# Optimization experiments

Measured on AMD Instinct MI355X. Metric: run time of the kernel, lower is better.

Reference implementation:

```python
import jax, jax.numpy as jnp
import numpy as np

N = 100000      # nodes
E = 3200000     # edges (before self loops)
F_IN = 5        # node_features
SH = 32         # spatial_hidden
H = 8           # heads
C = SH // H     # per-head dim = 4
TH = 64         # temporal_hidden
TC = TH // 3    # 21 (trend/seasonal lstm hidden)
TR = TH - 2 * TC  # 22 (residual mlp)
SEQ = 14
CV_THRESH = 1.5


def setup_inputs() -> dict:
    key = jax.random.key(0)
    cnt = [0]
    def nk():
        cnt[0] += 1
        return jax.random.fold_in(key, cnt[0])
    def nrm(shape, s=0.1):
        return jax.random.normal(nk(), shape, jnp.float32) * s
    inp = {}
    inp['x'] = nrm((N, F_IN), 1.0)
    inp['edge_index'] = jax.random.randint(nk(), (2, E), 0, N)
    inp['trend'] = nrm((1, SEQ), 1.0)
    inp['seasonal'] = nrm((1, SEQ), 1.0)
    inp['residual'] = nrm((1, SEQ), 1.0)
    inp['cv_values'] = jax.random.uniform(nk(), (1,), jnp.float32, 0.0, 3.0)
    inp['target_store_idx'] = 42
    # GAT layers: layer0 in=F_IN, layers 1,2 in=SH
    for i, din in enumerate([F_IN, SH, SH]):
        inp[f'gat_W{i}'] = nrm((din, SH), 1.0 / np.sqrt(din))
        inp[f'gat_as{i}'] = nrm((H, C))
        inp[f'gat_ad{i}'] = nrm((H, C))
        inp[f'gat_b{i}'] = jnp.zeros((SH,), jnp.float32)
    # two 2-layer LSTMs (input sizes 1 then TC), PyTorch gate order i,f,g,o
    for p in ('t', 's'):
        for l, din in enumerate([1, TC]):
            inp[f'{p}_Wih{l}'] = nrm((4 * TC, din), 1.0 / np.sqrt(TC))
            inp[f'{p}_Whh{l}'] = nrm((4 * TC, TC), 1.0 / np.sqrt(TC))
            inp[f'{p}_bih{l}'] = jnp.zeros((4 * TC,), jnp.float32)
            inp[f'{p}_bhh{l}'] = jnp.zeros((4 * TC,), jnp.float32)
    inp['res_W'] = nrm((1, TR), 1.0)
    inp['res_b'] = jnp.zeros((TR,), jnp.float32)
    FU = SH + TH  # 96
    inp['pg_W'] = nrm((FU + 1, FU), 1.0 / np.sqrt(FU))
    inp['pg_b'] = jnp.zeros((FU,), jnp.float32)
    inp['f1_W'] = nrm((FU, TH), 1.0 / np.sqrt(FU))
    inp['f1_b'] = jnp.zeros((TH,), jnp.float32)
    inp['ln_g'] = jnp.ones((TH,), jnp.float32)
    inp['ln_b'] = jnp.zeros((TH,), jnp.float32)
    inp['f2_W'] = nrm((TH, TH // 2), 1.0 / np.sqrt(TH))
    inp['f2_b'] = jnp.zeros((TH // 2,), jnp.float32)
    inp['f3_W'] = nrm((TH // 2, SEQ), 1.0 / np.sqrt(TH // 2))
    inp['f3_b'] = jnp.zeros((SEQ,), jnp.float32)
    return inp


def _gat(h_in, src, dst, W, a_s, a_d, b):
    # PyG GATConv: message src->dst, softmax over incoming edges per dst
    h = (h_in @ W).reshape(-1, H, C)            # [N,H,C]
    es = jnp.einsum('nhc,hc->nh', h, a_s)       # [N,H]
    ed = jnp.einsum('nhc,hc->nh', h, a_d)
    e = jax.nn.leaky_relu(es[src] + ed[dst], 0.2)  # [Etot,H]
    emax = jax.ops.segment_max(e, dst, num_segments=N)
    emax = jnp.where(jnp.isfinite(emax), emax, 0.0)
    a = jnp.exp(e - emax[dst])
    den = jax.ops.segment_sum(a, dst, num_segments=N)
    a = a / (den[dst] + 1e-16)
    out = jax.ops.segment_sum(h[src] * a[..., None], dst, num_segments=N)
    return out.reshape(-1, H * C) + b


def _lstm2(x, params):
    # x: [B,T,in]; params: list of (Wih[4h,in], Whh[4h,h], bih, bhh)
    seq = x
    for (Wih, Whh, bih, bhh) in params:
        B = seq.shape[0]
        hh = Whh.shape[1]
        def step(carry, xt):
            hprev, cprev = carry
            g = xt @ Wih.T + hprev @ Whh.T + bih + bhh
            i, f, gg, o = jnp.split(g, 4, axis=-1)
            c = jax.nn.sigmoid(f) * cprev + jax.nn.sigmoid(i) * jnp.tanh(gg)
            hn = jax.nn.sigmoid(o) * jnp.tanh(c)
            return (hn, c), hn
        init = (jnp.zeros((B, hh), seq.dtype), jnp.zeros((B, hh), seq.dtype))
        _, ys = jax.lax.scan(step, init, jnp.swapaxes(seq, 0, 1))
        seq = jnp.swapaxes(ys, 0, 1)
    return seq


def _forward(x, trend, seasonal, residual, cv_values,
             gat_params, lstm_t, lstm_s,
             res_W, res_b, pg_W, pg_b,
             f1_W, f1_b, ln_g, ln_b, f2_W, f2_b, f3_W, f3_b,
             edge_index, target_store_idx):
    loops = jnp.arange(N, dtype=edge_index.dtype)  # add_self_loops=True
    src = jnp.concatenate([edge_index[0], loops])
    dst = jnp.concatenate([edge_index[1], loops])
    h = x
    for (W, a_s, a_d, b) in gat_params:
        h = jax.nn.elu(_gat(h, src, dst, W, a_s, a_d, b))
    target_spatial = h[target_store_idx][None, :]          # [1,SH]
    trend_out = _lstm2(trend[..., None], lstm_t)[:, -1, :]      # [1,TC]
    seasonal_out = _lstm2(seasonal[..., None], lstm_s)[:, -1, :]
    res_out = jax.nn.relu(residual[..., None] @ res_W + res_b)[:, -1, :]  # [1,TR]
    temporal = jnp.concatenate([trend_out, seasonal_out, res_out], -1)    # [1,TH]
    combined = jnp.concatenate([target_spatial, temporal], -1)            # [1,96]
    gated_in = jnp.concatenate([combined, cv_values[:, None]], -1)        # [1,97]
    gate = jax.nn.sigmoid(gated_in @ pg_W + pg_b)
    gf = combined * gate
    h1 = gf @ f1_W + f1_b
    mu = h1.mean(-1, keepdims=True)
    var = h1.var(-1, keepdims=True)
    h1 = jax.nn.relu((h1 - mu) / jnp.sqrt(var + 1e-5) * ln_g + ln_b)
    h2 = jax.nn.relu(h1 @ f2_W + f2_b)
    return h2 @ f3_W + f3_b                                 # [1,SEQ]


def reference(x, edge_index, trend, seasonal, residual, cv_values, target_store_idx,
              gat_W0, gat_as0, gat_ad0, gat_b0,
              gat_W1, gat_as1, gat_ad1, gat_b1,
              gat_W2, gat_as2, gat_ad2, gat_b2,
              t_Wih0, t_Whh0, t_bih0, t_bhh0, t_Wih1, t_Whh1, t_bih1, t_bhh1,
              s_Wih0, s_Whh0, s_bih0, s_bhh0, s_Wih1, s_Whh1, s_bih1, s_bhh1,
              res_W, res_b, pg_W, pg_b,
              f1_W, f1_b, ln_g, ln_b, f2_W, f2_b, f3_W, f3_b):
    gat_params = [(gat_W0, gat_as0, gat_ad0, gat_b0),
                  (gat_W1, gat_as1, gat_ad1, gat_b1),
                  (gat_W2, gat_as2, gat_ad2, gat_b2)]
    lstm_t = [(t_Wih0, t_Whh0, t_bih0, t_bhh0), (t_Wih1, t_Whh1, t_bih1, t_bhh1)]
    lstm_s = [(s_Wih0, s_Whh0, s_bih0, s_bhh0), (s_Wih1, s_Whh1, s_bih1, s_bhh1)]
    return _forward(x, trend, seasonal, residual, cv_values,
                    gat_params, lstm_t, lstm_s,
                    res_W, res_b, pg_W, pg_b,
                    f1_W, f1_b, ln_g, ln_b, f2_W, f2_b, f3_W, f3_b,
                    edge_index, target_store_idx)
```

## Files before the change

### kernel.cpp

```cpp
#include <hip/hip_runtime.h>
#include <hip/hip_bf16.h>
#include <stdint.h>
#include <math.h>

#define NN   100000
#define EE   3200000
#define FIN  5
#define SHD  32
#define NH   8
#define TCH  21
#define TRH  22
#define SEQL 14

#define ECA   1024
#define ECL1  1024
#define ECB   16384
#define ECL2  8192
#define ECC   131072

#define BCHK2 4096
#define NBC2  ((EE + BCHK2 - 1) / BCHK2)
#define NBW   ((NN + 31) / 32)
#define NBWP  3200

typedef __hip_bfloat16 bf16;
typedef __attribute__((ext_vector_type(2))) float f32x2;

__device__ __forceinline__ float b2f(bf16 v) { return __bfloat162float(v); }
__device__ __forceinline__ float sigm(float x) { return 1.f / (1.f + __expf(-x)); }
__device__ __forceinline__ float ldw(const void* p, int i, int f) {
    return f ? ((const float*)p)[i] : __bfloat162float(((const bf16*)p)[i]);
}
__device__ __forceinline__ float relu_nan(float v) {
    return (v == v) ? ((v > 0.f) ? v : 0.f) : v;
}
__device__ __forceinline__ unsigned short f2b(float v) {
    bf16 b = __float2bfloat16(v);
    return *reinterpret_cast<unsigned short*>(&b);
}
__device__ __forceinline__ float cvf(float v) { return v; }
__device__ __forceinline__ float cvf(bf16 v) { return __bfloat162float(v); }
__device__ __forceinline__ void cp(float* dst, const void* src, int n,
                                   int t0, int stride, int f) {
    if (f) {
        const float* s = (const float*)src;
        for (int i = t0; i < n; i += stride) dst[i] = s[i];
    } else {
        const bf16* s = (const bf16*)src;
        for (int i = t0; i < n; i += stride) dst[i] = b2f(s[i]);
    }
}

__global__ void PatternAwareSTGAT_94489281309_kernel(const unsigned int* xw, int* flag,
        const void* as0, const void* b0, const void* as1, const void* b1,
        const void* as2, const void* b2, float* prm) {
    int tid = threadIdx.x;
    int sane = 0;
    for (int i = 0; i < 64; i++) {
        unsigned int lo = xw[i] & 0xFFFFu;
        int e = (int)((lo >> 7) & 0xFF);
        if (e >= 110 && e <= 135) sane++;
    }
    int f = (sane >= 32) ? 0 : 1;
    if (tid == 0) flag[0] = f;
    const void* asp[3] = {as0, as1, as2};
    const void* bp[3]  = {b0, b1, b2};
    for (int l = 0; l < 3; l++)
        prm[l * 64 + tid] = (tid < 32) ? ldw(asp[l], tid, f) : ldw(bp[l], tid - 32, f);
}

__global__ __launch_bounds__(256) void k_scan2(
        const int* __restrict__ ei, const unsigned* __restrict__ bm,
        const int* __restrict__ tgtp,
        int* __restrict__ es, int* __restrict__ edd,
        int* __restrict__ cnt, int* __restrict__ deg, int cap) {
    __shared__ unsigned sbm[NBWP];
    __shared__ int wsum[4];
    __shared__ int sbase;
    int tid = threadIdx.x;
    const bool useBm = (bm != nullptr);
    int tgtv = useBm ? -1 : tgtp[0];
    if (useBm) {
        const uint4* b4 = (const uint4*)bm;
        uint4* s4 = (uint4*)sbm;
        uint4 t0 = b4[tid];
        uint4 t1 = b4[tid + 256];
        uint4 t2 = (tid + 512 < NBWP / 4) ? b4[tid + 512] : make_uint4(0,0,0,0);
        uint4 t3 = (tid + 768 < NBWP / 4) ? b4[tid + 768] : make_uint4(0,0,0,0);
        s4[tid] = t0;
        s4[tid + 256] = t1;
        if (tid + 512 < NBWP / 4) s4[tid + 512] = t2;
        if (tid + 768 < NBWP / 4) s4[tid + 768] = t3;
    }
    __syncthreads();

    int e0 = blockIdx.x * BCHK2 + tid * 16;
    unsigned mask = 0;
    int dv[16];
    if (e0 < EE) {
        const int4* dd4 = (const int4*)(ei + EE + e0);
        int4 a = dd4[0];
        int4 b = dd4[1];
        int4 c = dd4[2];
        int4 d = dd4[3];
        dv[0]=a.x; dv[1]=a.y; dv[2]=a.z; dv[3]=a.w;
        dv[4]=b.x; dv[5]=b.y; dv[6]=b.z; dv[7]=b.w;
        dv[8]=c.x; dv[9]=c.y; dv[10]=c.z; dv[11]=c.w;
        dv[12]=d.x; dv[13]=d.y; dv[14]=d.z; dv[15]=d.w;
#pragma unroll
        for (int j = 0; j < 16; j++) {
            bool mm = useBm ? (((sbm[dv[j] >> 5] >> (dv[j] & 31)) & 1u) != 0u)
                            : (dv[j] == tgtv);
            if (mm) mask |= (1u << j);
        }
    }
    int m = __popc(mask);

    int lane = tid & 63, wv = tid >> 6;
    int pre = m;
#pragma unroll
    for (int off = 1; off < 64; off <<= 1) {
        int v = __shfl_up(pre, off, 64);
        if (lane >= off) pre += v;
    }
    if (lane == 63) wsum[wv] = pre;
    __syncthreads();
    int wbase = 0;
#pragma unroll
    for (int q = 0; q < 4; q++) if (q < wv) wbase += wsum[q];
    int myoff = wbase + pre - m;
    if (tid == 0) {
        int tot = wsum[0] + wsum[1] + wsum[2] + wsum[3];
        sbase = (tot > 0) ? atomicAdd(cnt, tot) : 0;
    }
    __syncthreads();
    if (m > 0) {
        int off = sbase + myoff;
#pragma unroll
        for (int j = 0; j < 16; j++) {
            if (mask & (1u << j)) {
                int e = e0 + j;
                int dval = dv[j];
                int s = ei[e];
                if (off < cap) { es[off] = s; edd[off] = dval; }
                if (deg) atomicAdd(&deg[dval], 1);
                off++;
            }
        }
    }
}

__global__ void k_mark1(const int* __restrict__ eA, const int* __restrict__ cA,
                        const int* __restrict__ tgtp,
                        unsigned* __restrict__ bm1, int* __restrict__ l1,
                        int* __restrict__ c1,
                        int* __restrict__ l3, int* __restrict__ c3) {
    int n = cA[0]; if (n > ECA) n = ECA;
    for (int i = threadIdx.x; i < n; i += 256) {
        int s = eA[i];
        unsigned bit = 1u << (s & 31);
        unsigned old = atomicOr(&bm1[s >> 5], bit);
        if (!(old & bit)) {
            int p = atomicAdd(c1, 1);
            if (p < ECL1) l1[p] = s;
        }
    }
    if (threadIdx.x == 0) {
        int t = tgtp[0];
        unsigned bit = 1u << (t & 31);
        unsigned old = atomicOr(&bm1[t >> 5], bit);
        if (!(old & bit)) {
            int p = atomicAdd(c1, 1);
            if (p < ECL1) l1[p] = t;
        }
        l3[0] = t; c3[0] = 1;
    }
}

__global__ void k_prefix(const int* __restrict__ list, const int* __restrict__ cp, int cap,
                         const int* __restrict__ deg, int* __restrict__ rstart,
                         unsigned* __restrict__ bmN, int* __restrict__ lN,
                         int* __restrict__ cN, int capN) {
    __shared__ int sdd[256];
    __shared__ int sbase;
    int n = cp[0]; if (n > cap) n = cap;
    if (threadIdx.x == 0) sbase = 0;
    __syncthreads();
    for (int b = 0; b < n; b += 256) {
        int i = b + threadIdx.x;
        int nd = (i < n) ? list[i] : -1;
        sdd[threadIdx.x] = (nd >= 0) ? deg[nd] : 0;
        __syncthreads();
        if (threadIdx.x == 0) {
            int acc = sbase;
            for (int j = 0; j < 256; j++) { int v = sdd[j]; sdd[j] = acc; acc += v; }
            sbase = acc;
        }
        __syncthreads();
        if (nd >= 0) rstart[nd] = sdd[threadIdx.x];
        __syncthreads();
    }
    if (bmN) {
        for (int i = threadIdx.x; i < n; i += 256) {
            int nd = list[i];
            unsigned bit = 1u << (nd & 31);
            unsigned old = atomicOr(&bmN[nd >> 5], bit);
            if (!(old & bit)) {
                int p = atomicAdd(cN, 1);
                if (p < capN) lN[p] = nd;
            }
        }
    }
}

__global__ __launch_bounds__(256) void k_scatter(const int* __restrict__ es,
                                                 const int* __restrict__ edd,
                                                 const int* __restrict__ cp, int cap,
                                                 const int* __restrict__ rstart,
                                                 int* __restrict__ fill, int* __restrict__ csr,
                                                 unsigned* __restrict__ bmN,
                                                 int* __restrict__ lN,
                                                 int* __restrict__ cN, int capN) {
    int m = cp[0]; if (m > cap) m = cap;
    for (int i = blockIdx.x * 256 + threadIdx.x; i < m; i += gridDim.x * 256) {
        int s = es[i], d = edd[i];
        int p = atomicAdd(&fill[d], 1);
        csr[rstart[d] + p] = s;
        if (bmN) {
            unsigned bit = 1u << (s & 31);
            unsigned old = atomicOr(&bmN[s >> 5], bit);
            if (!(old & bit)) {
                int q = atomicAdd(cN, 1);
                if (q < capN) lN[q] = s;
            }
        }
    }
}

__global__ void k_transform0(const void* x, const void* W, const void* ad_,
                             const int* flag, unsigned short* hWb, float* ed) {
    __shared__ float sW[FIN * SHD];
    __shared__ float sad[SHD];
    int tid = threadIdx.x;
    int f = flag[0];
    cp(sW, W, FIN * SHD, tid, 256, f);
    if (tid >= 192 && tid < 192 + SHD) sad[tid - 192] = ldw(ad_, tid - 192, f);
    __syncthreads();
    int n = blockIdx.x * 256 + tid;
    if (n >= NN) return;
    float xr[FIN];
    if (f) {
        const float* xp = (const float*)x + (size_t)n * FIN;
        for (int k = 0; k < FIN; k++) xr[k] = xp[k];
    } else {
        const bf16* xp = (const bf16*)x + (size_t)n * FIN;
        for (int k = 0; k < FIN; k++) xr[k] = b2f(xp[k]);
    }
    float o[SHD];
    for (int j = 0; j < SHD; j++) o[j] = 0.f;
    for (int k = 0; k < FIN; k++) {
        float xv = xr[k];
        for (int j = 0; j < SHD; j++) o[j] += xv * sW[k * SHD + j];
    }
    ushort4* row = (ushort4*)(hWb + (size_t)n * SHD);
    for (int q = 0; q < 8; q++) {
        ushort4 v; v.x = f2b(o[q*4]); v.y = f2b(o[q*4+1]); v.z = f2b(o[q*4+2]); v.w = f2b(o[q*4+3]);
        row[q] = v;
    }
    for (int h = 0; h < NH; h++) {
        float e2 = 0.f;
        for (int c = 0; c < 4; c++) e2 += o[h * 4 + c] * sad[h * 4 + c];
        ed[(size_t)n * NH + h] = e2;
    }
}

__global__ void k_transform1(const int* __restrict__ list, const int* __restrict__ cntp,
                             int cap,
                             const float* x, const void* W, const void* ad_,
                             const int* flag, unsigned short* hWb, float* ed) {
    __shared__ float sW[SHD * SHD];
    __shared__ float sad[SHD];
    int tid = threadIdx.x;
    int f = flag[0];
    cp(sW, W, SHD * SHD, tid, 256, f);
    if (tid >= 192 && tid < 192 + SHD) sad[tid - 192] = ldw(ad_, tid - 192, f);
    __syncthreads();
    int cnt = cntp[0]; if (cnt > cap) cnt = cap;
    int ii = blockIdx.x * 256 + tid;
    if (ii >= cnt) return;
    int n = list[ii];
    float xr[SHD];
    const float4* xp4 = (const float4*)(x + (size_t)n * SHD);
#pragma unroll
    for (int q = 0; q < 8; q++) {
        float4 v = xp4[q];
        xr[q*4] = v.x; xr[q*4+1] = v.y; xr[q*4+2] = v.z; xr[q*4+3] = v.w;
    }
    float o[SHD];
    for (int j = 0; j < SHD; j++) o[j] = 0.f;
    for (int k = 0; k < SHD; k++) {
        float xv = xr[k];
        for (int j = 0; j < SHD; j++) o[j] += xv * sW[k * SHD + j];
    }
    ushort4* row = (ushort4*)(hWb + (size_t)n * SHD);
    for (int q = 0; q < 8; q++) {
        ushort4 v; v.x = f2b(o[q*4]); v.y = f2b(o[q*4+1]); v.z = f2b(o[q*4+2]); v.w = f2b(o[q*4+3]);
        row[q] = v;
    }
    for (int h = 0; h < NH; h++) {
        float e2 = 0.f;
        for (int c = 0; c < 4; c++) e2 += o[h * 4 + c] * sad[h * 4 + c];
        ed[(size_t)n * NH + h] = e2;
    }
}

__global__ void k_aggregate(const int* __restrict__ list, const int* __restrict__ cntp,
                            int cap,
                            const int* __restrict__ rstart, const int* __restrict__ rdeg,
                            const int* __restrict__ csr,
                            const int* __restrict__ ovr, int ovrCap,
                            const unsigned short* __restrict__ hWb,
                            const float* __restrict__ ed,
                            const float* __restrict__ prm,
                            float* __restrict__ out) {
    int gid = blockIdx.x * 256 + threadIdx.x;
    int lane = threadIdx.x & 63;
    int cnt = cntp[0]; if (cnt > cap) cnt = cap;
    int idx = (gid >> 6) * 2 + (lane >> 5);
    if (idx >= cnt) return;
    int n = list[idx];
    int l32 = lane & 31;
    int h = l32 & 7, k = l32 >> 3;
    float4 asv = *(const float4*)(prm + h * 4);
    float ednh = ed[(size_t)n * NH + h];
    int base, deg;
    if (ovr) { base = 0; deg = ovr[0]; if (deg > ovrCap) deg = ovrCap; }
    else     { base = rstart[n]; deg = rdeg[n]; }
    float den = 0.f;
    f32x2 acc01 = {0.f, 0.f}, acc23 = {0.f, 0.f};
    int t = k;
    int s0 = -1, s1 = -1, s2 = -1, s3 = -1, s4 = -1, s5 = -1;
    if (t <= deg)      s0 = (t == 0) ? n : __builtin_nontemporal_load(csr + base + t - 1);
    if (t + 4 <= deg)  s1 = __builtin_nontemporal_load(csr + base + t + 3);
    if (t + 8 <= deg)  s2 = __builtin_nontemporal_load(csr + base + t + 7);
    if (t + 12 <= deg) s3 = __builtin_nontemporal_load(csr + base + t + 11);
    if (t + 16 <= deg) s4 = __builtin_nontemporal_load(csr + base + t + 15);
    if (t + 20 <= deg) s5 = __builtin_nontemporal_load(csr + base + t + 19);
    while (s0 >= 0) {
        uint2 hv0 = *(const uint2*)(hWb + (size_t)s0 * SHD + h * 4);
        bool b1 = (s1 >= 0), b2 = (s2 >= 0), b3 = (s3 >= 0), b4 = (s4 >= 0), b5 = (s5 >= 0);
        uint2 hv1, hv2, hv3, hv4, hv5;
        if (b1) hv1 = *(const uint2*)(hWb + (size_t)s1 * SHD + h * 4);
        if (b2) hv2 = *(const uint2*)(hWb + (size_t)s2 * SHD + h * 4);
        if (b3) hv3 = *(const uint2*)(hWb + (size_t)s3 * SHD + h * 4);
        if (b4) hv4 = *(const uint2*)(hWb + (size_t)s4 * SHD + h * 4);
        if (b5) hv5 = *(const uint2*)(hWb + (size_t)s5 * SHD + h * 4);
        int tn = t + 24;
        int p0 = -1, p1 = -1, p2 = -1, p3 = -1, p4 = -1, p5 = -1;
        if (tn <= deg)      p0 = __builtin_nontemporal_load(csr + base + tn - 1);
        if (tn + 4 <= deg)  p1 = __builtin_nontemporal_load(csr + base + tn + 3);
        if (tn + 8 <= deg)  p2 = __builtin_nontemporal_load(csr + base + tn + 7);
        if (tn + 12 <= deg) p3 = __builtin_nontemporal_load(csr + base + tn + 11);
        if (tn + 16 <= deg) p4 = __builtin_nontemporal_load(csr + base + tn + 15);
        if (tn + 20 <= deg) p5 = __builtin_nontemporal_load(csr + base + tn + 19);
        {
            f32x2 h01, h23;
            h01.x = __uint_as_float(hv0.x << 16);
            h01.y = __uint_as_float(hv0.x & 0xffff0000u);
            h23.x = __uint_as_float(hv0.y << 16);
            h23.y = __uint_as_float(hv0.y & 0xffff0000u);
            f32x2 d2 = h01 * (f32x2){asv.x, asv.y} + h23 * (f32x2){asv.z, asv.w};
            float e = d2.x + d2.y + ednh;
            e = fmaxf(e, 0.2f * e);
            float a = __expf(e);
            den += a;
            f32x2 av = {a, a};
            acc01 += av * h01;
            acc23 += av * h23;
        }
        if (b1) {
            f32x2 h01, h23;
            h01.x = __uint_as_float(hv1.x << 16);
            h01.y = __uint_as_float(hv1.x & 0xffff0000u);
            h23.x = __uint_as_float(hv1.y << 16);
            h23.y = __uint_as_float(hv1.y & 0xffff0000u);
            f32x2 d2 = h01 * (f32x2){asv.x, asv.y} + h23 * (f32x2){asv.z, asv.w};
            float e = d2.x + d2.y + ednh;
            e = fmaxf(e, 0.2f * e);
            float a = __expf(e);
            den += a;
            f32x2 av = {a, a};
            acc01 += av * h01;
            acc23 += av * h23;
        }
        if (b2) {
            f32x2 h01, h23;
            h01.x = __uint_as_float(hv2.x << 16);
            h01.y = __uint_as_float(hv2.x & 0xffff0000u);
            h23.x = __uint_as_float(hv2.y << 16);
            h23.y = __uint_as_float(hv2.y & 0xffff0000u);
            f32x2 d2 = h01 * (f32x2){asv.x, asv.y} + h23 * (f32x2){asv.z, asv.w};
            float e = d2.x + d2.y + ednh;
            e = fmaxf(e, 0.2f * e);
            float a = __expf(e);
            den += a;
            f32x2 av = {a, a};
            acc01 += av * h01;
            acc23 += av * h23;
        }
        if (b3) {
            f32x2 h01, h23;
            h01.x = __uint_as_float(hv3.x << 16);
            h01.y = __uint_as_float(hv3.x & 0xffff0000u);
            h23.x = __uint_as_float(hv3.y << 16);
            h23.y = __uint_as_float(hv3.y & 0xffff0000u);
            f32x2 d2 = h01 * (f32x2){asv.x, asv.y} + h23 * (f32x2){asv.z, asv.w};
            float e = d2.x + d2.y + ednh;
            e = fmaxf(e, 0.2f * e);
            float a = __expf(e);
            den += a;
            f32x2 av = {a, a};
            acc01 += av * h01;
            acc23 += av * h23;
        }
        if (b4) {
            f32x2 h01, h23;
            h01.x = __uint_as_float(hv4.x << 16);
            h01.y = __uint_as_float(hv4.x & 0xffff0000u);
            h23.x = __uint_as_float(hv4.y << 16);
            h23.y = __uint_as_float(hv4.y & 0xffff0000u);
            f32x2 d2 = h01 * (f32x2){asv.x, asv.y} + h23 * (f32x2){asv.z, asv.w};
            float e = d2.x + d2.y + ednh;
            e = fmaxf(e, 0.2f * e);
            float a = __expf(e);
            den += a;
            f32x2 av = {a, a};
            acc01 += av * h01;
            acc23 += av * h23;
        }
        if (b5) {
            f32x2 h01, h23;
            h01.x = __uint_as_float(hv5.x << 16);
            h01.y = __uint_as_float(hv5.x & 0xffff0000u);
            h23.x = __uint_as_float(hv5.y << 16);
            h23.y = __uint_as_float(hv5.y & 0xffff0000u);
            f32x2 d2 = h01 * (f32x2){asv.x, asv.y} + h23 * (f32x2){asv.z, asv.w};
            float e = d2.x + d2.y + ednh;
            e = fmaxf(e, 0.2f * e);
            float a = __expf(e);
            den += a;
            f32x2 av = {a, a};
            acc01 += av * h01;
            acc23 += av * h23;
        }
        s0 = p0; s1 = p1; s2 = p2; s3 = p3; s4 = p4; s5 = p5; t = tn;
    }
    for (int off = 16; off >= 8; off >>= 1) {
        den      += __shfl_down(den, off, 32);
        acc01.x  += __shfl_down(acc01.x, off, 32);
        acc01.y  += __shfl_down(acc01.y, off, 32);
        acc23.x  += __shfl_down(acc23.x, off, 32);
        acc23.y  += __shfl_down(acc23.y, off, 32);
    }
    if (k == 0) {
        float inv = 1.f / (den + 1e-16f);
        float4 bv = *(const float4*)(prm + 32 + h * 4);
        float v0 = acc01.x * inv + bv.x;
        float v1 = acc01.y * inv + bv.y;
        float v2 = acc23.x * inv + bv.z;
        float v3 = acc23.y * inv + bv.w;
        v0 = (v0 > 0.f) ? v0 : expm1f(v0);
        v1 = (v1 > 0.f) ? v1 : expm1f(v1);
        v2 = (v2 > 0.f) ? v2 : expm1f(v2);
        v3 = (v3 > 0.f) ? v3 : expm1f(v3);
        *(float4*)(out + (size_t)n * SHD + h * 4) = make_float4(v0, v1, v2, v3);
    }
}

template<typename T>
__device__ __forceinline__ void lstm_load_regs(
        const T* Wih0, const T* Whh0, const T* bih0, const T* bhh0,
        const T* Wih1, const T* Whh1, const T* bih1, const T* bhh1,
        const T* xin, int l, bool bl, float* xs,
        float& wa, float& ba, float& wb, float& bb, float& ba2, float& bb2,
        float* Wa, float* Wb, float* Ua, float* Va, float* Ub, float* Vb) {
#pragma unroll
    for (int t = 0; t < SEQL; t++) xs[t] = cvf(xin[t]);
    wa = cvf(Wih0[l]);
    ba = cvf(bih0[l]) + cvf(bhh0[l]);
    wb = bl ? cvf(Wih0[64 + l]) : 0.f;
    bb = bl ? (cvf(bih0[64 + l]) + cvf(bhh0[64 + l])) : 0.f;
    ba2 = cvf(bih1[l]) + cvf(bhh1[l]);
    bb2 = bl ? (cvf(bih1[64 + l]) + cvf(bhh1[64 + l])) : 0.f;
#pragma unroll
    for (int j = 0; j < 21; j++) {
        Wa[j] = cvf(Whh0[l * 21 + j]);
        Wb[j] = bl ? cvf(Whh0[(64 + l) * 21 + j]) : 0.f;
        Ua[j] = cvf(Wih1[l * 21 + j]);
        Va[j] = cvf(Whh1[l * 21 + j]);
        Ub[j] = bl ? cvf(Wih1[(64 + l) * 21 + j]) : 0.f;
        Vb[j] = bl ? cvf(Whh1[(64 + l) * 21 + j]) : 0.f;
    }
}

__device__ __forceinline__ void warm_sweep(const void* p, int nbytes, int t2) {
    const uint4* s = (const uint4*)p;
    int nv = nbytes >> 4;
    unsigned acc = 0;
    for (int i = t2; i < nv; i += 1024) {
        uint4 v0 = s[i];
        uint4 v1 = (i + 128 < nv) ? s[i + 128] : make_uint4(0,0,0,0);
        uint4 v2 = (i + 256 < nv) ? s[i + 256] : make_uint4(0,0,0,0);
        uint4 v3 = (i + 384 < nv) ? s[i + 384] : make_uint4(0,0,0,0);
        uint4 v4 = (i + 512 < nv) ? s[i + 512] : make_uint4(0,0,0,0);
        uint4 v5 = (i + 640 < nv) ? s[i + 640] : make_uint4(0,0,0,0);
        uint4 v6 = (i + 768 < nv) ? s[i + 768] : make_uint4(0,0,0,0);
        uint4 v7 = (i + 896 < nv) ? s[i + 896] : make_uint4(0,0,0,0);
        acc ^= v0.x ^ v1.x ^ v2.x ^ v3.x ^ v4.x ^ v5.x ^ v6.x ^ v7.x;
    }
    asm volatile("" :: "v"(acc));
}

template<typename T>
__device__ __forceinline__ float matvec_t(const T* W, const float* vin,
                                          float bias, int n, int col, int ncol) {
    float acc = bias;
    int k2 = 0;
    for (; k2 + 8 <= n; k2 += 8) {
        float w0 = cvf(W[(k2 + 0) * ncol + col]);
        float w1 = cvf(W[(k2 + 1) * ncol + col]);
        float w2 = cvf(W[(k2 + 2) * ncol + col]);
        float w3 = cvf(W[(k2 + 3) * ncol + col]);
        float w4 = cvf(W[(k2 + 4) * ncol + col]);
        float w5 = cvf(W[(k2 + 5) * ncol + col]);
        float w6 = cvf(W[(k2 + 6) * ncol + col]);
        float w7 = cvf(W[(k2 + 7) * ncol + col]);
        acc += vin[k2 + 0] * w0; acc += vin[k2 + 1] * w1;
        acc += vin[k2 + 2] * w2; acc += vin[k2 + 3] * w3;
        acc += vin[k2 + 4] * w4; acc += vin[k2 + 5] * w5;
        acc += vin[k2 + 6] * w6; acc += vin[k2 + 7] * w7;
    }
    for (; k2 < n; k2++) acc += vin[k2] * cvf(W[k2 * ncol + col]);
    return acc;
}
__device__ __forceinline__ float matvec(const void* W, const float* vin,
                                        float bias, int n, int col, int ncol, int f) {
    return f ? matvec_t<float>((const float*)W, vin, bias, n, col, ncol)
             : matvec_t<bf16>((const bf16*)W, vin, bias, n, col, ncol);
}

__global__ __launch_bounds__(256, 1)
void k_tail(const void* trend, const void* seasonal, const void* residual,
                       const void* cv, const int* tgtp,
                       const void* tWih0, const void* tWhh0, const void* tbih0, const void* tbhh0,
                       const void* tWih1, const void* tWhh1, const void* tbih1, const void* tbhh1,
                       const void* sWih0, const void* sWhh0, const void* sbih0, const void* sbhh0,
                       const void* sWih1, const void* sWhh1, const void* sbih1, const void* sbhh1,
                       const void* res_W, const void* res_b,
                       const void* pg_W, const void* pg_b,
                       const void* f1_W, const void* f1_b,
                       const void* ln_g, const void* ln_b,
                       const void* f2_W, const void* f2_b,
                       const void* f3_W, const void* f3_b,
                       const int* flag, const float* A, void* out) {
    __shared__ __align__(16) float SH1[2][24];
    __shared__ __align__(16) float SH2[2][24];
    __shared__ float comb[97];
    __shared__ float gf[96];
    __shared__ float h1v[64];
    __shared__ float h2s[32];
    __shared__ float sbias[336];
    __shared__ float stats[2];
    const int tid = threadIdx.x;
    const int f = flag[0];
    const int w = tid >> 6, l = tid & 63;

    if (tid < 96) {
        if (tid < 48) SH1[tid / 24][tid % 24] = 0.f;
        else { int u = tid - 48; SH2[u / 24][u % 24] = 0.f; }
    }
    __syncthreads();

    if (w < 2) {
        const void* Wih0 = w ? sWih0 : tWih0;
        const void* Whh0 = w ? sWhh0 : tWhh0;
        const void* bih0 = w ? sbih0 : tbih0;
        const void* bhh0 = w ? sbhh0 : tbhh0;
        const void* Wih1 = w ? sWih1 : tWih1;
        const void* Whh1 = w ? sWhh1 : tWhh1;
        const void* bih1 = w ? sbih1 : tbih1;
        const void* bhh1 = w ? sbhh1 : tbhh1;
        const void* xin  = w ? seasonal : trend;
        const bool bl = (l < 20);
        float xs[SEQL];
        float wa, ba, wb, bb, ba2, bb2;
        float Wa[21], Wb[21], Ua[21], Va[21], Ub[21], Vb[21];
        if (f) {
            lstm_load_regs<float>((const float*)Wih0, (const float*)Whh0,
                (const float*)bih0, (const float*)bhh0,
                (const float*)Wih1, (const float*)Whh1,
                (const float*)bih1, (const float*)bhh1,
                (const float*)xin, l, bl, xs, wa, ba, wb, bb, ba2, bb2,
                Wa, Wb, Ua, Va, Ub, Vb);
        } else {
            lstm_load_regs<bf16>((const bf16*)Wih0, (const bf16*)Whh0,
                (const bf16*)bih0, (const bf16*)bhh0,
                (const bf16*)Wih1, (const bf16*)Whh1,
                (const bf16*)bih1, (const bf16*)bhh1,
                (const bf16*)xin, l, bl, xs, wa, ba, wb, bb, ba2, bb2,
                Wa, Wb, Ua, Va, Ub, Vb);
        }
#pragma unroll
        for (int j = 0; j < 21; j++) {
            asm volatile("" : "+v"(Wa[j]), "+v"(Wb[j]));
            asm volatile("" : "+v"(Ua[j]), "+v"(Va[j]));
            asm volatile("" : "+v"(Ub[j]), "+v"(Vb[j]));
        }
#pragma unroll
        for (int t = 0; t < SEQL; t++) asm volatile("" : "+v"(xs[t]));
        asm volatile("" : "+v"(wa), "+v"(ba));
        asm volatile("" : "+v"(wb), "+v"(bb));
        asm volatile("" : "+v"(ba2), "+v"(bb2));

        float h1r = 0.f, c1v = 0.f, h2r = 0.f, c2v = 0.f;
#pragma unroll 1
        for (int t = 0; t < SEQL; t++) {
            float aa = ba + xs[t] * wa;
            float ab = bb + xs[t] * wb;
#pragma unroll
            for (int q = 0; q < 5; q++) {
                float4 v = *(const float4*)&SH1[w][q * 4];
                aa += v.x * Wa[q*4];   ab += v.x * Wb[q*4];
                aa += v.y * Wa[q*4+1]; ab += v.y * Wb[q*4+1];
                aa += v.z * Wa[q*4+2]; ab += v.z * Wb[q*4+2];
                aa += v.w * Wa[q*4+3]; ab += v.w * Wb[q*4+3];
            }
            { float v20 = SH1[w][20]; aa += v20 * Wa[20]; ab += v20 * Wb[20]; }
            float fj = __shfl(aa, 21 + l);
            float gj = __shfl(aa, 42 + l);
            float oa = __shfl(aa, 63);
            float ob = __shfl(ab, (l == 0) ? 0 : (l - 1));
            float oj = (l == 0) ? oa : ob;
            if (l < 21) {
                c1v = sigm(fj) * c1v + sigm(aa) * tanhf(gj);
                h1r = sigm(oj) * tanhf(c1v);
                SH1[w][l] = h1r;
            }
            __threadfence_block();
            float a2 = ba2, b2v = bb2;
#pragma unroll
            for (int q = 0; q < 5; q++) {
                float4 u = *(const float4*)&SH1[w][q * 4];
                float4 v = *(const float4*)&SH2[w][q * 4];
                a2  += u.x * Ua[q*4]   + v.x * Va[q*4];
                b2v += u.x * Ub[q*4]   + v.x * Vb[q*4];
                a2  += u.y * Ua[q*4+1] + v.y * Va[q*4+1];
                b2v += u.y * Ub[q*4+1] + v.y * Vb[q*4+1];
                a2  += u.z * Ua[q*4+2] + v.z * Va[q*4+2];
                b2v += u.z * Ub[q*4+2] + v.z * Vb[q*4+2];
                a2  += u.w * Ua[q*4+3] + v.w * Va[q*4+3];
                b2v += u.w * Ub[q*4+3] + v.w * Vb[q*4+3];
            }
            { float u20 = SH1[w][20], v20 = SH2[w][20];
              a2  += u20 * Ua[20] + v20 * Va[20];
              b2v += u20 * Ub[20] + v20 * Vb[20]; }
            float fj2 = __shfl(a2, 21 + l);
            float gj2 = __shfl(a2, 42 + l);
            float oa2 = __shfl(a2, 63);
            float ob2 = __shfl(b2v, (l == 0) ? 0 : (l - 1));
            float oj2 = (l == 0) ? oa2 : ob2;
            if (l < 21) {
                c2v = sigm(fj2) * c2v + sigm(a2) * tanhf(gj2);
                h2r = sigm(oj2) * tanhf(c2v);
                SH2[w][l] = h2r;
            }
            __threadfence_block();
        }
        if (l < 21) comb[(w == 0 ? 32 : 53) + l] = h2r;
    } else {
        int t2 = tid - 128;
        if (t2 < TRH)
            comb[74 + t2] = relu_nan(ldw(residual, SEQL - 1, f) * ldw(res_W, t2, f)
                                     + ldw(res_b, t2, f));
        if (t2 == TRH) comb[96] = ldw(cv, 0, f);
        if (t2 >= 32 && t2 < 64) {
            int tgt = tgtp[0];
            comb[t2 - 32] = A[(size_t)tgt * SHD + (t2 - 32)];
        }
        for (int i = t2; i < 336; i += 128) {
            float v;
            if (i < 96)       v = ldw(pg_b, i, f);
            else if (i < 160) v = ldw(f1_b, i - 96, f);
            else if (i < 192) v = ldw(f2_b, i - 160, f);
            else if (i < 206) v = ldw(f3_b, i - 192, f);
            else if (i < 208) v = 0.f;
            else if (i < 272) v = ldw(ln_g, i - 208, f);
            else              v = ldw(ln_b, i - 272, f);
            sbias[i] = v;
        }
        int esz = f ? 4 : 2;
        warm_sweep(pg_W, 9312 * esz, t2);
        warm_sweep(f1_W, 6144 * esz, t2);
        warm_sweep(f2_W, 2048 * esz, t2);
        warm_sweep(f3_W,  448 * esz, t2);
    }
    __syncthreads();

    if (tid < 96)
        gf[tid] = comb[tid] * sigm(matvec(pg_W, comb, sbias[tid], 97, tid, 96, f));
    __syncthreads();
    if (tid < 64)
        h1v[tid] = matvec(f1_W, gf, sbias[96 + tid], 96, tid, 64, f);
    __syncthreads();
    if (tid == 0) {
        float mu = 0.f;
        for (int j = 0; j < 64; j++) mu += h1v[j];
        mu /= 64.f;
        float var = 0.f;
        for (int j = 0; j < 64; j++) { float d = h1v[j] - mu; var += d * d; }
        var /= 64.f;
        stats[0] = mu; stats[1] = rsqrtf(var + 1e-5f);
    }
    __syncthreads();
    if (tid < 64)
        h1v[tid] = relu_nan((h1v[tid] - stats[0]) * stats[1] * sbias[208 + tid] + sbias[272 + tid]);
    __syncthreads();
    if (tid < 32)
        h2s[tid] = relu_nan(matvec(f2_W, h1v, sbias[160 + tid], 64, tid, 32, f));
    __syncthreads();
    if (tid < SEQL) {
        float acc = matvec(f3_W, h2s, sbias[192 + tid], 32, tid, 14, f);
        if (acc != acc) acc = 3333.0f;
        if (f) ((float*)out)[tid] = acc;
        else   ((bf16*)out)[tid] = __float2bfloat16(acc);
    }
}

static inline unsigned short h_f2bf(float f) {
    union { float f; unsigned u; } x; x.f = f;
    return (unsigned short)(x.u >> 16);
}
static unsigned short g_diag[SEQL];

extern "C" void kernel_launch(void* const* d_in, const int* in_sizes, int n_in,
                              void* d_out, int out_size, void* d_ws, size_t ws_size,
                              hipStream_t stream) {
    const int* ei  = (const int*)d_in[1];
    const int* tgt = (const int*)d_in[6];

    const size_t HWB  = sizeof(unsigned short) * (size_t)NN * SHD;
    const size_t EDB  = sizeof(float) * (size_t)NN * NH;
    const size_t AB   = sizeof(float) * (size_t)NN * SHD;
    const size_t ZER  = sizeof(int) * (size_t)(16 + 2 * NBWP + 4 * NN);
    const size_t RSTB = sizeof(int) * (size_t)(2 * NN);
    const size_t LSTB = sizeof(int) * (size_t)(2 * ECA + ECL1 + 8 + ECL2
                                               + 3 * ECB + 3 * ECC);
    const size_t NEED = 256 + 1024 + ZER + RSTB + LSTB + 512 + HWB + EDB + AB;
    if (ws_size < NEED) {
        for (int i = 0; i < SEQL; i++) g_diag[i] = h_f2bf(7777.0f);
        hipMemcpyAsync(d_out, g_diag, SEQL * sizeof(unsigned short),
                       hipMemcpyHostToDevice, stream);
        return;
    }

    char* p = (char*)d_ws;
    int*   flag = (int*)p;   p += 256;
    float* prm  = (float*)p; p += 1024;
    int* cnts  = (int*)p; p += sizeof(int) * 16;
    unsigned* bm1 = (unsigned*)p; p += sizeof(int) * NBWP;
    unsigned* bm2 = (unsigned*)p; p += sizeof(int) * NBWP;
    int* degB  = (int*)p; p += sizeof(int) * NN;
    int* fillB = (int*)p; p += sizeof(int) * NN;
    int* degC  = (int*)p; p += sizeof(int) * NN;
    int* fillC = (int*)p; p += sizeof(int) * NN;
    int* rstartB = (int*)p; p += sizeof(int) * NN;
    int* rstartC = (int*)p; p += sizeof(int) * NN;
    int* eA   = (int*)p; p += sizeof(int) * ECA;
    int* eAd  = (int*)p; p += sizeof(int) * ECA;
    int* l1   = (int*)p; p += sizeof(int) * ECL1;
    int* l3   = (int*)p; p += sizeof(int) * 8;
    int* l2   = (int*)p; p += sizeof(int) * ECL2;
    int* eBs  = (int*)p; p += sizeof(int) * ECB;
    int* eBd  = (int*)p; p += sizeof(int) * ECB;
    int* csrB = (int*)p; p += sizeof(int) * ECB;
    int* eCs  = (int*)p; p += sizeof(int) * ECC;
    int* eCd  = (int*)p; p += sizeof(int) * ECC;
    int* csrC = (int*)p; p += sizeof(int) * ECC;
    p = (char*)(((uintptr_t)p + 255) & ~(uintptr_t)255);
    unsigned short* hWb = (unsigned short*)p; p += HWB;
    float* ed = (float*)p; p += EDB;
    float* A  = (float*)p; p += AB;
    int* cA = cnts; int* c1 = cnts + 1; int* cB = cnts + 2;
    int* c2 = cnts + 3; int* cC = cnts + 4; int* c3 = cnts + 5;

    dim3 b256(256);
    dim3 gN((NN + 255) / 256);
    dim3 gScan(NBC2);

    PatternAwareSTGAT_94489281309_kernel<<<dim3(1), dim3(64), 0, stream>>>(
        (const unsigned int*)d_in[0], flag,
        d_in[8], d_in[10], d_in[12], d_in[14], d_in[16], d_in[18], prm);

    hipMemsetAsync(cnts, 0, ZER, stream);

    k_scan2<<<gScan, b256, 0, stream>>>(ei, (const unsigned*)nullptr, tgt,
                                        eA, eAd, cA, (int*)nullptr, ECA);
    k_mark1<<<dim3(1), b256, 0, stream>>>(eA, cA, tgt, bm1, l1, c1, l3, c3);
    k_scan2<<<gScan, b256, 0, stream>>>(ei, bm1, tgt, eBs, eBd, cB, degB, ECB);
    k_prefix<<<dim3(1), b256, 0, stream>>>(l1, c1, ECL1, degB, rstartB,
                                           bm2, l2, c2, ECL2);
    k_scatter<<<dim3(64), b256, 0, stream>>>(eBs, eBd, cB, ECB, rstartB, fillB, csrB,
                                             bm2, l2, c2, ECL2);
    k_scan2<<<gScan, b256, 0, stream>>>(ei, bm2, tgt, eCs, eCd, cC, degC, ECC);
    k_prefix<<<dim3(1), b256, 0, stream>>>(l2, c2, ECL2, degC, rstartC,
                                           (unsigned*)nullptr, (int*)nullptr,
                                           (int*)nullptr, 0);
    k_scatter<<<dim3(512), b256, 0, stream>>>(eCs, eCd, cC, ECC, rstartC, fillC, csrC,
                                              (unsigned*)nullptr, (int*)nullptr,
                                              (int*)nullptr, 0);

    k_transform0<<<gN, b256, 0, stream>>>(d_in[0], d_in[7], d_in[9], flag, hWb, ed);
    k_aggregate<<<dim3(ECL2 * 32 / 256), b256, 0, stream>>>(l2, c2, ECL2,
        rstartC, degC, csrC, (const int*)nullptr, 0, hWb, ed, prm, A);
    k_transform1<<<dim3(ECL2 / 256), b256, 0, stream>>>(l2, c2, ECL2,
        A, d_in[11], d_in[13], flag, hWb, ed);
    k_aggregate<<<dim3(ECL1 * 32 / 256), b256, 0, stream>>>(l1, c1, ECL1,
        rstartB, degB, csrB, (const int*)nullptr, 0, hWb, ed, prm + 64, A);
    k_transform1<<<dim3((ECL1 + 255) / 256), b256, 0, stream>>>(l1, c1, ECL1,
        A, d_in[15], d_in[17], flag, hWb, ed);
    k_aggregate<<<dim3(1), b256, 0, stream>>>(l3, c3, 8,
        (const int*)nullptr, (const int*)nullptr, eA, cA, ECA, hWb, ed, prm + 128, A);

    k_tail<<<dim3(1), b256, 0, stream>>>(
        d_in[2], d_in[3], d_in[4], d_in[5], tgt,
        d_in[19], d_in[20], d_in[21], d_in[22],
        d_in[23], d_in[24], d_in[25], d_in[26],
        d_in[27], d_in[28], d_in[29], d_in[30],
        d_in[31], d_in[32], d_in[33], d_in[34],
        d_in[35], d_in[36],
        d_in[37], d_in[38],
        d_in[39], d_in[40],
        d_in[41], d_in[42],
        d_in[43], d_in[44],
        d_in[45], d_in[46],
        flag, A, d_out);
}
```

Before: 296.0 us.

## Replace compacted CSR build with fixed-stride per-node rows and fused frontier scans

Neighbor lists for the 1- and 2-hop frontiers are now written into fixed-stride per-node row buffers (96 slots per node) indexed by an atomic fill counter. This replaces the compact-edge, degree, prefix-sum and scatter passes. The first scan also marks the 1-hop and 2-hop bitmaps directly, which removes k_mark1, both k_prefix launches and both k_scatter launches, leaving three full edge scans and no serial single-block prefix steps. The cost is a much larger workspace (two NN×96 int buffers) and silent truncation for any node with more than 96 in-edges. Per-edge atomics also replace the block-aggregated counter atomic.

```diff
diff --git a/kernel.cpp b/kernel.cpp
--- a/kernel.cpp
+++ b/kernel.cpp
@@ -14,9 +14,8 @@
 
 #define ECA   1024
 #define ECL1  1024
-#define ECB   16384
 #define ECL2  8192
-#define ECC   131072
+#define RSTR  96
 
 #define BCHK2 4096
 #define NBC2  ((EE + BCHK2 - 1) / BCHK2)
@@ -69,18 +68,58 @@
         prm[l * 64 + tid] = (tid < 32) ? ldw(asp[l], tid, f) : ldw(bp[l], tid - 32, f);
 }
 
-__global__ __launch_bounds__(256) void k_scan2(
+__global__ __launch_bounds__(256) void k_scanA(
+        const int* __restrict__ ei, const int* __restrict__ tgtp,
+        int* __restrict__ eA, int* __restrict__ cA,
+        unsigned* __restrict__ bm1, int* __restrict__ l1, int* __restrict__ c1,
+        unsigned* __restrict__ bm2, int* __restrict__ l2, int* __restrict__ c2,
+        int* __restrict__ l3, int* __restrict__ c3) {
+    int tid = threadIdx.x;
+    int tgtv = tgtp[0];
+    if (blockIdx.x == 0 && tid == 0) {
+        unsigned bit = 1u << (tgtv & 31);
+        unsigned old = atomicOr(&bm1[tgtv >> 5], bit);
+        if (!(old & bit)) { int p = atomicAdd(c1, 1); if (p < ECL1) l1[p] = tgtv; }
+        old = atomicOr(&bm2[tgtv >> 5], bit);
+        if (!(old & bit)) { int p = atomicAdd(c2, 1); if (p < ECL2) l2[p] = tgtv; }
+        l3[0] = tgtv; c3[0] = 1;
+    }
+    int e0 = blockIdx.x * BCHK2 + tid * 16;
+    if (e0 >= EE) return;
+    const int4* dd4 = (const int4*)(ei + EE + e0);
+    int4 a = dd4[0], b = dd4[1], c = dd4[2], d = dd4[3];
+    int dv[16];
+    dv[0]=a.x; dv[1]=a.y; dv[2]=a.z; dv[3]=a.w;
+    dv[4]=b.x; dv[5]=b.y; dv[6]=b.z; dv[7]=b.w;
+    dv[8]=c.x; dv[9]=c.y; dv[10]=c.z; dv[11]=c.w;
+    dv[12]=d.x; dv[13]=d.y; dv[14]=d.z; dv[15]=d.w;
+    unsigned mask = 0;
+#pragma unroll
+    for (int j = 0; j < 16; j++) if (dv[j] == tgtv) mask |= (1u << j);
+    if (!mask) return;
+#pragma unroll
+    for (int j = 0; j < 16; j++) {
+        if (mask & (1u << j)) {
+            int s = ei[e0 + j];
+            int p = atomicAdd(cA, 1);
+            if (p < ECA) eA[p] = s;
+            unsigned bit = 1u << (s & 31);
+            unsigned old = atomicOr(&bm1[s >> 5], bit);
+            if (!(old & bit)) { int q = atomicAdd(c1, 1); if (q < ECL1) l1[q] = s; }
+            old = atomicOr(&bm2[s >> 5], bit);
+            if (!(old & bit)) { int q = atomicAdd(c2, 1); if (q < ECL2) l2[q] = s; }
+        }
+    }
+}
+
+__global__ __launch_bounds__(256) void k_scanR(
         const int* __restrict__ ei, const unsigned* __restrict__ bm,
-        const int* __restrict__ tgtp,
-        int* __restrict__ es, int* __restrict__ edd,
-        int* __restrict__ cnt, int* __restrict__ deg, int cap) {
+        int* __restrict__ fill, int* __restrict__ rows,
+        unsigned* __restrict__ bmN, int* __restrict__ lN,
+        int* __restrict__ cN, int capN) {
     __shared__ unsigned sbm[NBWP];
-    __shared__ int wsum[4];
-    __shared__ int sbase;
     int tid = threadIdx.x;
-    const bool useBm = (bm != nullptr);
-    int tgtv = useBm ? -1 : tgtp[0];
-    if (useBm) {
+    {
         const uint4* b4 = (const uint4*)bm;
         uint4* s4 = (uint4*)sbm;
         uint4 t0 = b4[tid];
@@ -93,145 +132,34 @@
         if (tid + 768 < NBWP / 4) s4[tid + 768] = t3;
     }
     __syncthreads();
-
     int e0 = blockIdx.x * BCHK2 + tid * 16;
+    if (e0 >= EE) return;
+    const int4* dd4 = (const int4*)(ei + EE + e0);
+    int4 a = dd4[0], b = dd4[1], c = dd4[2], d = dd4[3];
+    int dv[16];
+    dv[0]=a.x; dv[1]=a.y; dv[2]=a.z; dv[3]=a.w;
+    dv[4]=b.x; dv[5]=b.y; dv[6]=b.z; dv[7]=b.w;
+    dv[8]=c.x; dv[9]=c.y; dv[10]=c.z; dv[11]=c.w;
+    dv[12]=d.x; dv[13]=d.y; dv[14]=d.z; dv[15]=d.w;
     unsigned mask = 0;
-    int dv[16];
-    if (e0 < EE) {
-        const int4* dd4 = (const int4*)(ei + EE + e0);
-        int4 a = dd4[0];
-        int4 b = dd4[1];
-        int4 c = dd4[2];
-        int4 d = dd4[3];
-        dv[0]=a.x; dv[1]=a.y; dv[2]=a.z; dv[3]=a.w;
-        dv[4]=b.x; dv[5]=b.y; dv[6]=b.z; dv[7]=b.w;
-        dv[8]=c.x; dv[9]=c.y; dv[10]=c.z; dv[11]=c.w;
-        dv[12]=d.x; dv[13]=d.y; dv[14]=d.z; dv[15]=d.w;
-#pragma unroll
-        for (int j = 0; j < 16; j++) {
-            bool mm = useBm ? (((sbm[dv[j] >> 5] >> (dv[j] & 31)) & 1u) != 0u)
-                            : (dv[j] == tgtv);
-            if (mm) mask |= (1u << j);
-        }
-    }
-    int m = __popc(mask);
-
-    int lane = tid & 63, wv = tid >> 6;
-    int pre = m;
-#pragma unroll
-    for (int off = 1; off < 64; off <<= 1) {
-        int v = __shfl_up(pre, off, 64);
-        if (lane >= off) pre += v;
-    }
-    if (lane == 63) wsum[wv] = pre;
-    __syncthreads();
-    int wbase = 0;
-#pragma unroll
-    for (int q = 0; q < 4; q++) if (q < wv) wbase += wsum[q];
-    int myoff = wbase + pre - m;
-    if (tid == 0) {
-        int tot = wsum[0] + wsum[1] + wsum[2] + wsum[3];
-        sbase = (tot > 0) ? atomicAdd(cnt, tot) : 0;
-    }
-    __syncthreads();
-    if (m > 0) {
-        int off = sbase + myoff;
-#pragma unroll
-        for (int j = 0; j < 16; j++) {
-            if (mask & (1u << j)) {
-                int e = e0 + j;
-                int dval = dv[j];
-                int s = ei[e];
-                if (off < cap) { es[off] = s; edd[off] = dval; }
-                if (deg) atomicAdd(&deg[dval], 1);
-                off++;
-            }
-        }
-    }
-}
-
-__global__ void k_mark1(const int* __restrict__ eA, const int* __restrict__ cA,
-                        const int* __restrict__ tgtp,
-                        unsigned* __restrict__ bm1, int* __restrict__ l1,
-                        int* __restrict__ c1,
-                        int* __restrict__ l3, int* __restrict__ c3) {
-    int n = cA[0]; if (n > ECA) n = ECA;
-    for (int i = threadIdx.x; i < n; i += 256) {
-        int s = eA[i];
-        unsigned bit = 1u << (s & 31);
-        unsigned old = atomicOr(&bm1[s >> 5], bit);
-        if (!(old & bit)) {
-            int p = atomicAdd(c1, 1);
-            if (p < ECL1) l1[p] = s;
-        }
-    }
-    if (threadIdx.x == 0) {
-        int t = tgtp[0];
-        unsigned bit = 1u << (t & 31);
-        unsigned old = atomicOr(&bm1[t >> 5], bit);
-        if (!(old & bit)) {
-            int p = atomicAdd(c1, 1);
-            if (p < ECL1) l1[p] = t;
-        }
-        l3[0] = t; c3[0] = 1;
-    }
-}
-
-__global__ void k_prefix(const int* __restrict__ list, const int* __restrict__ cp, int cap,
-                         const int* __restrict__ deg, int* __restrict__ rstart,
-                         unsigned* __restrict__ bmN, int* __restrict__ lN,
-                         int* __restrict__ cN, int capN) {
-    __shared__ int sdd[256];
-    __shared__ int sbase;
-    int n = cp[0]; if (n > cap) n = cap;
-    if (threadIdx.x == 0) sbase = 0;
-    __syncthreads();
-    for (int b = 0; b < n; b += 256) {
-        int i = b + threadIdx.x;
-        int nd = (i < n) ? list[i] : -1;
-        sdd[threadIdx.x] = (nd >= 0) ? deg[nd] : 0;
-        __syncthreads();
-        if (threadIdx.x == 0) {
-            int acc = sbase;
-            for (int j = 0; j < 256; j++) { int v = sdd[j]; sdd[j] = acc; acc += v; }
-            sbase = acc;
-        }
-        __syncthreads();
-        if (nd >= 0) rstart[nd] = sdd[threadIdx.x];
-        __syncthreads();
-    }
-    if (bmN) {
-        for (int i = threadIdx.x; i < n; i += 256) {
-            int nd = list[i];
-            unsigned bit = 1u << (nd & 31);
-            unsigned old = atomicOr(&bmN[nd >> 5], bit);
-            if (!(old & bit)) {
-                int p = atomicAdd(cN, 1);
-                if (p < capN) lN[p] = nd;
-            }
-        }
-    }
-}
-
-__global__ __launch_bounds__(256) void k_scatter(const int* __restrict__ es,
-                                                 const int* __restrict__ edd,
-                                                 const int* __restrict__ cp, int cap,
-                                                 const int* __restrict__ rstart,
-                                                 int* __restrict__ fill, int* __restrict__ csr,
-                                                 unsigned* __restrict__ bmN,
-                                                 int* __restrict__ lN,
-                                                 int* __restrict__ cN, int capN) {
-    int m = cp[0]; if (m > cap) m = cap;
-    for (int i = blockIdx.x * 256 + threadIdx.x; i < m; i += gridDim.x * 256) {
-        int s = es[i], d = edd[i];
-        int p = atomicAdd(&fill[d], 1);
-        csr[rstart[d] + p] = s;
-        if (bmN) {
-            unsigned bit = 1u << (s & 31);
-            unsigned old = atomicOr(&bmN[s >> 5], bit);
-            if (!(old & bit)) {
-                int q = atomicAdd(cN, 1);
-                if (q < capN) lN[q] = s;
+#pragma unroll
+    for (int j = 0; j < 16; j++)
+        if ((sbm[dv[j] >> 5] >> (dv[j] & 31)) & 1u) mask |= (1u << j);
+    if (!mask) return;
+#pragma unroll
+    for (int j = 0; j < 16; j++) {
+        if (mask & (1u << j)) {
+            int dn = dv[j];
+            int s = ei[e0 + j];
+            int p = atomicAdd(&fill[dn], 1);
+            if (p < RSTR) rows[(size_t)dn * RSTR + p] = s;
+            if (bmN) {
+                unsigned bit = 1u << (s & 31);
+                unsigned old = atomicOr(&bmN[s >> 5], bit);
+                if (!(old & bit)) {
+                    int q = atomicAdd(cN, 1);
+                    if (q < capN) lN[q] = s;
+                }
             }
         }
     }
@@ -316,7 +244,7 @@
 
 __global__ void k_aggregate(const int* __restrict__ list, const int* __restrict__ cntp,
                             int cap,
-                            const int* __restrict__ rstart, const int* __restrict__ rdeg,
+                            const int* __restrict__ rdeg,
                             const int* __restrict__ csr,
                             const int* __restrict__ ovr, int ovrCap,
                             const unsigned short* __restrict__ hWb,
@@ -335,7 +263,7 @@
     float ednh = ed[(size_t)n * NH + h];
     int base, deg;
     if (ovr) { base = 0; deg = ovr[0]; if (deg > ovrCap) deg = ovrCap; }
-    else     { base = rstart[n]; deg = rdeg[n]; }
+    else     { base = n * RSTR; deg = rdeg[n]; if (deg > RSTR) deg = RSTR; }
     float den = 0.f;
     f32x2 acc01 = {0.f, 0.f}, acc23 = {0.f, 0.f};
     int t = k;
@@ -751,11 +679,10 @@
     const size_t HWB  = sizeof(unsigned short) * (size_t)NN * SHD;
     const size_t EDB  = sizeof(float) * (size_t)NN * NH;
     const size_t AB   = sizeof(float) * (size_t)NN * SHD;
-    const size_t ZER  = sizeof(int) * (size_t)(16 + 2 * NBWP + 4 * NN);
-    const size_t RSTB = sizeof(int) * (size_t)(2 * NN);
-    const size_t LSTB = sizeof(int) * (size_t)(2 * ECA + ECL1 + 8 + ECL2
-                                               + 3 * ECB + 3 * ECC);
-    const size_t NEED = 256 + 1024 + ZER + RSTB + LSTB + 512 + HWB + EDB + AB;
+    const size_t ZER  = sizeof(int) * (size_t)(16 + 2 * NBWP + 2 * NN);
+    const size_t ROWB = sizeof(int) * (size_t)NN * RSTR;
+    const size_t LSTB = sizeof(int) * (size_t)(ECA + ECL1 + 8 + ECL2);
+    const size_t NEED = 256 + 1024 + ZER + LSTB + 2 * ROWB + 512 + HWB + EDB + AB;
     if (ws_size < NEED) {
         for (int i = 0; i < SEQL; i++) g_diag[i] = h_f2bf(7777.0f);
         hipMemcpyAsync(d_out, g_diag, SEQL * sizeof(unsigned short),
@@ -769,29 +696,19 @@
     int* cnts  = (int*)p; p += sizeof(int) * 16;
     unsigned* bm1 = (unsigned*)p; p += sizeof(int) * NBWP;
     unsigned* bm2 = (unsigned*)p; p += sizeof(int) * NBWP;
-    int* degB  = (int*)p; p += sizeof(int) * NN;
     int* fillB = (int*)p; p += sizeof(int) * NN;
-    int* degC  = (int*)p; p += sizeof(int) * NN;
     int* fillC = (int*)p; p += sizeof(int) * NN;
-    int* rstartB = (int*)p; p += sizeof(int) * NN;
-    int* rstartC = (int*)p; p += sizeof(int) * NN;
     int* eA   = (int*)p; p += sizeof(int) * ECA;
-    int* eAd  = (int*)p; p += sizeof(int) * ECA;
     int* l1   = (int*)p; p += sizeof(int) * ECL1;
     int* l3   = (int*)p; p += sizeof(int) * 8;
     int* l2   = (int*)p; p += sizeof(int) * ECL2;
-    int* eBs  = (int*)p; p += sizeof(int) * ECB;
-    int* eBd  = (int*)p; p += sizeof(int) * ECB;
-    int* csrB = (int*)p; p += sizeof(int) * ECB;
-    int* eCs  = (int*)p; p += sizeof(int) * ECC;
-    int* eCd  = (int*)p; p += sizeof(int) * ECC;
-    int* csrC = (int*)p; p += sizeof(int) * ECC;
+    int* rowsB = (int*)p; p += ROWB;
+    int* rowsC = (int*)p; p += ROWB;
     p = (char*)(((uintptr_t)p + 255) & ~(uintptr_t)255);
     unsigned short* hWb = (unsigned short*)p; p += HWB;
     float* ed = (float*)p; p += EDB;
     float* A  = (float*)p; p += AB;
-    int* cA = cnts; int* c1 = cnts + 1; int* cB = cnts + 2;
-    int* c2 = cnts + 3; int* cC = cnts + 4; int* c3 = cnts + 5;
+    int* cA = cnts; int* c1 = cnts + 1; int* c2 = cnts + 2; int* c3 = cnts + 3;
 
     dim3 b256(256);
     dim3 gN((NN + 255) / 256);
@@ -803,33 +720,25 @@
 
     hipMemsetAsync(cnts, 0, ZER, stream);
 
-    k_scan2<<<gScan, b256, 0, stream>>>(ei, (const unsigned*)nullptr, tgt,
-                                        eA, eAd, cA, (int*)nullptr, ECA);
-    k_mark1<<<dim3(1), b256, 0, stream>>>(eA, cA, tgt, bm1, l1, c1, l3, c3);
-    k_scan2<<<gScan, b256, 0, stream>>>(ei, bm1, tgt, eBs, eBd, cB, degB, ECB);
-    k_prefix<<<dim3(1), b256, 0, stream>>>(l1, c1, ECL1, degB, rstartB,
-                                           bm2, l2, c2, ECL2);
-    k_scatter<<<dim3(64), b256, 0, stream>>>(eBs, eBd, cB, ECB, rstartB, fillB, csrB,
-                                             bm2, l2, c2, ECL2);
-    k_scan2<<<gScan, b256, 0, stream>>>(ei, bm2, tgt, eCs, eCd, cC, degC, ECC);
-    k_prefix<<<dim3(1), b256, 0, stream>>>(l2, c2, ECL2, degC, rstartC,
-                                           (unsigned*)nullptr, (int*)nullptr,
-                                           (int*)nullptr, 0);
-    k_scatter<<<dim3(512), b256, 0, stream>>>(eCs, eCd, cC, ECC, rstartC, fillC, csrC,
-                                              (unsigned*)nullptr, (int*)nullptr,
-                                              (int*)nullptr, 0);
+    k_scanA<<<gScan, b256, 0, stream>>>(ei, tgt, eA, cA,
+                                        bm1, l1, c1, bm2, l2, c2, l3, c3);
+    k_scanR<<<gScan, b256, 0, stream>>>(ei, bm1, fillB, rowsB,
+                                        bm2, l2, c2, ECL2);
+    k_scanR<<<gScan, b256, 0, stream>>>(ei, bm2, fillC, rowsC,
+                                        (unsigned*)nullptr, (int*)nullptr,
+                                        (int*)nullptr, 0);
 
     k_transform0<<<gN, b256, 0, stream>>>(d_in[0], d_in[7], d_in[9], flag, hWb, ed);
     k_aggregate<<<dim3(ECL2 * 32 / 256), b256, 0, stream>>>(l2, c2, ECL2,
-        rstartC, degC, csrC, (const int*)nullptr, 0, hWb, ed, prm, A);
+        fillC, rowsC, (const int*)nullptr, 0, hWb, ed, prm, A);
     k_transform1<<<dim3(ECL2 / 256), b256, 0, stream>>>(l2, c2, ECL2,
         A, d_in[11], d_in[13], flag, hWb, ed);
     k_aggregate<<<dim3(ECL1 * 32 / 256), b256, 0, stream>>>(l1, c1, ECL1,
-        rstartB, degB, csrB, (const int*)nullptr, 0, hWb, ed, prm + 64, A);
+        fillB, rowsB, (const int*)nullptr, 0, hWb, ed, prm + 64, A);
     k_transform1<<<dim3((ECL1 + 255) / 256), b256, 0, stream>>>(l1, c1, ECL1,
         A, d_in[15], d_in[17], flag, hWb, ed);
     k_aggregate<<<dim3(1), b256, 0, stream>>>(l3, c3, 8,
-        (const int*)nullptr, (const int*)nullptr, eA, cA, ECA, hWb, ed, prm + 128, A);
+        (const int*)nullptr, eA, cA, ECA, hWb, ed, prm + 128, A);
 
     k_tail<<<dim3(1), b256, 0, stream>>>(
         d_in[2], d_in[3], d_in[4], d_in[5], tgt,
```

New measurement: 255.6 us. -13.7%, faster.
